# Kernel optimization log

Hardware: AMD Instinct MI355X
Metric: run time of the kernel (lower is better)

## Reference

```python
import jax, jax.numpy as jnp
import numpy as np

NEG_SLOPE = 0.2

def setup_inputs() -> dict:
    key = jax.random.key(0)
    ks = jax.random.split(key, 10)
    N, E, L, D, H = 100000, 3200000, 200000, 128, 128
    x = jax.random.normal(ks[0], (N, D), dtype=jnp.float32)
    edge_index = jax.random.randint(ks[1], (2, E), 0, N, dtype=jnp.int64)
    edge_label_index = jax.random.randint(ks[2], (2, L), 0, N, dtype=jnp.int64)
    s = 1.0 / np.sqrt(D)
    W1l = jax.random.uniform(ks[3], (D, H), minval=-s, maxval=s, dtype=jnp.float32)
    b1 = jax.random.uniform(ks[4], (H,), minval=-s, maxval=s, dtype=jnp.float32)
    W1r = jax.random.uniform(ks[5], (D, H), minval=-s, maxval=s, dtype=jnp.float32)
    s2 = 1.0 / np.sqrt(H)
    W2l = jax.random.uniform(ks[6], (H, H), minval=-s2, maxval=s2, dtype=jnp.float32)
    b2 = jax.random.uniform(ks[7], (H,), minval=-s2, maxval=s2, dtype=jnp.float32)
    W2r = jax.random.uniform(ks[8], (H, H), minval=-s2, maxval=s2, dtype=jnp.float32)
    return {"x": x, "edge_index": edge_index, "edge_label_index": edge_label_index,
            "W1l": W1l, "b1": b1, "W1r": W1r, "W2l": W2l, "b2": b2, "W2r": W2r}

def reference(x, edge_index, edge_label_index, W1l, b1, W1r, W2l, b2, W2r):
    N = x.shape[0]
    src, dst = edge_index[0], edge_index[1]
    # in-degree for mean aggregation (clamped to avoid div-by-zero, matching mean over empty = 0)
    deg = jax.ops.segment_sum(jnp.ones_like(dst, dtype=x.dtype), dst, num_segments=N)
    inv_deg = (1.0 / jnp.maximum(deg, 1.0))[:, None]

    def sage(h, Wl, b, Wr):
        # mean of source-node features over incoming edges at each target node
        agg = jax.ops.segment_sum(h[src], dst, num_segments=N) * inv_deg
        return agg @ Wl + b + h @ Wr

    h = sage(x, W1l, b1, W1r)
    h = jnp.where(h >= 0, h, NEG_SLOPE * h)  # leaky_relu; eval mode so no dropout
    h = sage(h, W2l, b2, W2r)
    x_src = h[edge_label_index[0]]
    x_trg = h[edge_label_index[1]]
    return jnp.sum(x_src * x_trg, axis=1)
```

## Files before the change

kernel.cpp:

```cpp
#include <hip/hip_runtime.h>
#include <hip/hip_fp16.h>


#define D128 128
#define BSHIFT 9
#define BNODES 512

typedef __bf16 bf16x8 __attribute__((ext_vector_type(8)));
typedef float  f32x4  __attribute__((ext_vector_type(4)));
typedef _Float16 h2   __attribute__((ext_vector_type(2)));

union uh2cast { unsigned u; h2 h; };
__device__ inline h2 uash2(unsigned u) { uh2cast c; c.u = u; return c.h; }

__device__ inline unsigned short f2bf(float f) {
    unsigned u = __float_as_uint(f);
    u = u + 0x7FFF + ((u >> 16) & 1);
    return (unsigned short)(u >> 16);
}
__device__ inline float bf2f(unsigned short s) {
    return __uint_as_float(((unsigned)s) << 16);
}
__device__ inline unsigned packbf2(float lo, float hi) {
    return (unsigned)f2bf(lo) | ((unsigned)f2bf(hi) << 16);
}
__device__ inline unsigned char f2e5(float f) {
    unsigned short h = __half_as_ushort(__float2half(f));
    h = (unsigned short)(h + 0x7F + ((h >> 8) & 1));
    return (unsigned char)(h >> 8);
}


__global__ void prep_kernel(const float* __restrict__ in, unsigned short* __restrict__ outb,
                            unsigned char* __restrict__ out8, int n4,
                            const float* __restrict__ W1l, const float* __restrict__ W1r,
                            const float* __restrict__ W2l, const float* __restrict__ W2r,
                            unsigned short* __restrict__ packed,
                            const int* __restrict__ dst, int* __restrict__ bh,
                            int E, int castBlocks, int histBlocks) {
    int bid = blockIdx.x;
    int t = threadIdx.x;
    if (bid < castBlocks) {
        int i = bid * 256 + t;
        if (i >= n4) return;
        float4 v = ((const float4*)in)[i];
        ushort4 ob;
        ob.x = f2bf(v.x); ob.y = f2bf(v.y); ob.z = f2bf(v.z); ob.w = f2bf(v.w);
        ((ushort4*)outb)[i] = ob;
        unsigned p = (unsigned)f2e5(v.x) | ((unsigned)f2e5(v.y) << 8) |
                     ((unsigned)f2e5(v.z) << 16) | ((unsigned)f2e5(v.w) << 24);
        ((unsigned*)out8)[i] = p;
    } else if (bid < castBlocks + 256) {
        int tid = (bid - castBlocks) * 256 + t;
        int layer = tid >> 15;
        int r = tid & 32767;
        int j    = r & 7;
        int lane = (r >> 3) & 63;
        int nt   = (r >> 9) & 7;
        int kc   = (r >> 12) & 7;
        int k   = kc * 32 + ((lane >> 4) << 3) + j;
        int col = nt * 16 + (lane & 15);
        const float* Wl = layer ? W2l : W1l;
        const float* Wr = layer ? W2r : W1r;
        float v = (k < 128) ? Wl[k * 128 + col] : Wr[(k - 128) * 128 + col];
        packed[tid] = f2bf(v);
    } else {
        __shared__ int h[256];
        int hb = bid - castBlocks - 256;
        if (hb >= histBlocks) return;
        h[t] = 0;
        __syncthreads();
        int base = hb * 8192;
#pragma unroll
        for (int k = 0; k < 32; ++k) {
            int e = base + k * 256 + t;
            if (e < E) atomicAdd(&h[dst[e] >> BSHIFT], 1);
        }
        __syncthreads();
        bh[hb * 256 + t] = h[t];
    }
}


__global__ void bucket_scan(const int* __restrict__ bh, int nhb,
                            int* __restrict__ bucket_base, int* __restrict__ bucket_cur,
                            int* __restrict__ rowptr, int NB, int N, int E) {
    __shared__ int sc[256];
    __shared__ int orig[256];
    int t = threadIdx.x;
    int v = 0;
    for (int b = 0; b < nhb; ++b) v += bh[b * 256 + t];
    if (t >= NB) v = 0;
    orig[t] = v;
    sc[t] = v;
    __syncthreads();
    for (int off = 1; off < 256; off <<= 1) {
        int a = (t >= off) ? sc[t - off] : 0;
        __syncthreads();
        sc[t] += a;
        __syncthreads();
    }
    int ex = sc[t] - orig[t];
    if (t < NB) { bucket_base[t] = ex; bucket_cur[t] = ex; }
    if (t == 0) { bucket_base[NB] = E; rowptr[N] = E; }
}

__global__ void scatter_kernel(const int* __restrict__ src, const int* __restrict__ dst,
                               int* __restrict__ bucket_cur, int* __restrict__ pairs,
                               int E, int NB) {
    __shared__ int hist[256], lscan[256], gbase[256];
    __shared__ int lsrc[1024], ldst[1024];
    int t = threadIdx.x;
    hist[t] = 0;
    __syncthreads();
    int base = blockIdx.x * 1024;
    int total = E - base; if (total > 1024) total = 1024;

    int ms[4], md[4], mb[4], mr[4];
#pragma unroll
    for (int k = 0; k < 4; ++k) {
        int i = k * 256 + t;
        int e = base + i;
        mb[k] = -1;
        if (i < total) {
            ms[k] = src[e];
            md[k] = dst[e];
            mb[k] = md[k] >> BSHIFT;
            mr[k] = atomicAdd(&hist[mb[k]], 1);
        }
    }
    __syncthreads();
    lscan[t] = hist[t];
    __syncthreads();
    for (int off = 1; off < 256; off <<= 1) {
        int a = (t >= off) ? lscan[t - off] : 0;
        __syncthreads();
        lscan[t] += a;
        __syncthreads();
    }
    lscan[t] -= hist[t];
    if (t < NB && hist[t] > 0) gbase[t] = atomicAdd(&bucket_cur[t], hist[t]);
    __syncthreads();
#pragma unroll
    for (int k = 0; k < 4; ++k) {
        if (mb[k] >= 0) {
            int idx = lscan[mb[k]] + mr[k];
            lsrc[idx] = ms[k];
            ldst[idx] = md[k];
        }
    }
    __syncthreads();
#pragma unroll
    for (int k = 0; k < 4; ++k) {
        int i = k * 256 + t;
        if (i < total) {
            int d = ldst[i];
            int b = d >> BSHIFT;
            int pos = gbase[b] + (i - lscan[b]);
            pairs[pos] = (lsrc[i] << BSHIFT) | (d & (BNODES - 1));
        }
    }
}

__global__ void bucket_fill(const int* __restrict__ pairs, const int* __restrict__ bucket_base,
                            int* __restrict__ rowptr, int* __restrict__ srcs, int N) {
    __shared__ int hist[BNODES], excl[BNODES], sc[BNODES];
    int b = blockIdx.x;
    int t = threadIdx.x;
    int node0 = b << BSHIFT;
    int pbeg = bucket_base[b];
    int pend = bucket_base[b + 1];
    hist[t] = 0;
    __syncthreads();
    for (int p = pbeg + t; p < pend; p += BNODES) {
        atomicAdd(&hist[pairs[p] & (BNODES - 1)], 1);
    }
    __syncthreads();
    sc[t] = hist[t];
    __syncthreads();
    for (int off = 1; off < BNODES; off <<= 1) {
        int a = (t >= off) ? sc[t - off] : 0;
        __syncthreads();
        sc[t] += a;
        __syncthreads();
    }
    excl[t] = sc[t] - hist[t];
    int node = node0 + t;
    if (node < N) rowptr[node] = pbeg + excl[t];
    __syncthreads();
    hist[t] = 0;
    __syncthreads();
    for (int p = pbeg + t; p < pend; p += BNODES) {
        int w = pairs[p];
        int dl = w & (BNODES - 1);
        int c = atomicAdd(&hist[dl], 1);
        srcs[pbeg + excl[dl] + c] = (int)(((unsigned)w) >> BSHIFT) << 4;
    }
}


__device__ inline void pkacc8(h2* A, uint2 v) {
    A[0] += uash2((v.x << 8) & 0xFF00FF00u);
    A[1] += uash2(v.x & 0xFF00FF00u);
    A[2] += uash2((v.y << 8) & 0xFF00FF00u);
    A[3] += uash2(v.y & 0xFF00FF00u);
}

__global__ void agg_kernel(const int* __restrict__ rowptr, const int* __restrict__ srcs,
                           const unsigned char* __restrict__ feat8,
                           unsigned short* __restrict__ out, int N) {
    int wave = threadIdx.x >> 6;
    int lane = threadIdx.x & 63;
    int q  = lane >> 4;
    int ql = lane & 15;
    int n = blockIdx.x * 4 + wave;
    if (n >= N) return;
    int beg = rowptr[n];
    int end = rowptr[n + 1];
    const uint2* f = (const uint2*)feat8;

    h2 A0[4], A1[4], A2[4], A3[4];
    h2 z; z[0] = (_Float16)0.f; z[1] = (_Float16)0.f;
#pragma unroll
    for (int k = 0; k < 4; ++k) { A0[k] = z; A1[k] = z; A2[k] = z; A3[k] = z; }

    int j = beg;
    int pre = (4 - (beg & 3)) & 3;
    if (pre > end - beg) pre = end - beg;
    if (q < pre) {
        uint2 v = f[srcs[j + q] + ql];
        pkacc8(A1, v);
    }
    j += pre;

    for (; j + 16 <= end; j += 16) {
        int4 e = *(const int4*)(srcs + j + 4 * q);
        uint2 v0 = f[e.x + ql];
        uint2 v1 = f[e.y + ql];
        uint2 v2 = f[e.z + ql];
        uint2 v3 = f[e.w + ql];
        pkacc8(A0, v0);
        pkacc8(A1, v1);
        pkacc8(A2, v2);
        pkacc8(A3, v3);
    }
    for (; j + 4 <= end; j += 4) {
        uint2 v = f[srcs[j + q] + ql];
        pkacc8(A0, v);
    }
    int rem = end - j;
    if (q < rem) {
        uint2 v = f[srcs[j + q] + ql];
        pkacc8(A2, v);
    }

    float c[8];
#pragma unroll
    for (int p = 0; p < 4; ++p) {
        float lo = (float)A0[p][0] + (float)A1[p][0] + (float)A2[p][0] + (float)A3[p][0];
        float hi = (float)A0[p][1] + (float)A1[p][1] + (float)A2[p][1] + (float)A3[p][1];
        int base = (p >> 1) * 4 + (p & 1);
        c[base] = lo;
        c[base + 2] = hi;
    }

#pragma unroll
    for (int k = 0; k < 8; ++k) {
        c[k] += __shfl_xor(c[k], 16, 64);
        c[k] += __shfl_xor(c[k], 32, 64);
    }

    int deg = end - beg;
    float inv = deg > 0 ? 1.0f / (float)deg : 0.f;
    if (q == 0) {
        uint4 r;
        r.x = packbf2(c[0] * inv, c[1] * inv);
        r.y = packbf2(c[2] * inv, c[3] * inv);
        r.z = packbf2(c[4] * inv, c[5] * inv);
        r.w = packbf2(c[6] * inv, c[7] * inv);
        ((uint4*)out)[(size_t)n * 16 + ql] = r;
    }
}


template <bool LEAKY>
__global__ void mm_kernel(const unsigned short* __restrict__ A,
                          const unsigned short* __restrict__ F,
                          const unsigned short* __restrict__ Wp,
                          const float* __restrict__ bias,
                          unsigned short* __restrict__ out,
                          unsigned char* __restrict__ out8, int N) {
    int wid = threadIdx.x >> 6;
    int lane = threadIdx.x & 63;
    int quad = lane >> 4;
    int m0 = (blockIdx.x * 4 + wid) * 32;

    int rowA0 = m0 + (lane & 15);
    int rowA1 = rowA0 + 16;
    if (rowA0 > N - 1) rowA0 = N - 1;
    if (rowA1 > N - 1) rowA1 = N - 1;

    f32x4 acc[2][8];
#pragma unroll
    for (int t = 0; t < 2; ++t)
#pragma unroll
        for (int nt = 0; nt < 8; ++nt) acc[t][nt] = (f32x4){0.f, 0.f, 0.f, 0.f};

#pragma unroll
    for (int kc = 0; kc < 8; ++kc) {
        const unsigned short* src = (kc < 4) ? (A + kc * 32) : (F + (kc - 4) * 32);
        bf16x8 af0 = *(const bf16x8*)(src + (size_t)rowA0 * D128 + quad * 8);
        bf16x8 af1 = *(const bf16x8*)(src + (size_t)rowA1 * D128 + quad * 8);
        const unsigned short* wp = Wp + ((size_t)kc * 8) * 512 + lane * 8;
#pragma unroll
        for (int nt = 0; nt < 8; ++nt) {
            bf16x8 bf = *(const bf16x8*)(wp + nt * 512);
            acc[0][nt] = __builtin_amdgcn_mfma_f32_16x16x32_bf16(af0, bf, acc[0][nt], 0, 0, 0);
            acc[1][nt] = __builtin_amdgcn_mfma_f32_16x16x32_bf16(af1, bf, acc[1][nt], 0, 0, 0);
        }
    }

#pragma unroll
    for (int nt = 0; nt < 8; ++nt) {
        int col = nt * 16 + (lane & 15);
        float bv = bias[col];
#pragma unroll
        for (int t = 0; t < 2; ++t) {
#pragma unroll
            for (int r = 0; r < 4; ++r) {
                int row = m0 + t * 16 + quad * 4 + r;
                if (row < N) {
                    float v = acc[t][nt][r] + bv;
                    if (LEAKY) v = v >= 0.f ? v : 0.2f * v;
                    out[(size_t)row * D128 + col] = f2bf(v);
                    if (out8) out8[(size_t)row * D128 + col] = f2e5(v);
                }
            }
        }
    }
}


__global__ void score_kernel(const int* __restrict__ eli, const unsigned short* __restrict__ h,
                             float* __restrict__ out, int L) {
    int wave = threadIdx.x >> 6;
    int lane = threadIdx.x & 63;
    int l0 = (blockIdx.x * 4 + wave) * 4;
    if (l0 >= L) return;
    const ushort2* h2p = (const ushort2*)h;
    int a[4], b[4];
#pragma unroll
    for (int k = 0; k < 4; ++k) {
        int l = l0 + k;
        if (l > L - 1) l = L - 1;
        a[k] = eli[l];
        b[k] = eli[L + l];
    }
    float p[4];
#pragma unroll
    for (int k = 0; k < 4; ++k) {
        ushort2 u = h2p[(size_t)a[k] * 64 + lane];
        ushort2 v = h2p[(size_t)b[k] * 64 + lane];
        p[k] = bf2f(u.x) * bf2f(v.x) + bf2f(u.y) * bf2f(v.y);
    }
#pragma unroll
    for (int off = 32; off > 0; off >>= 1) {
#pragma unroll
        for (int k = 0; k < 4; ++k) p[k] += __shfl_down(p[k], off, 64);
    }
    if (lane == 0) {
#pragma unroll
        for (int k = 0; k < 4; ++k) {
            if (l0 + k < L) out[l0 + k] = p[k];
        }
    }
}


extern "C" void kernel_launch(void* const* d_in, const int* in_sizes, int n_in,
                              void* d_out, int out_size, void* d_ws, size_t ws_size,
                              hipStream_t stream) {
    const float* x   = (const float*)d_in[0];
    const int*   ei  = (const int*)d_in[1];
    const int*   eli = (const int*)d_in[2];
    const float* W1l = (const float*)d_in[3];
    const float* b1  = (const float*)d_in[4];
    const float* W1r = (const float*)d_in[5];
    const float* W2l = (const float*)d_in[6];
    const float* b2  = (const float*)d_in[7];
    const float* W2r = (const float*)d_in[8];

    const int N = in_sizes[0] / D128;
    const int E = in_sizes[1] / 2;
    const int L = in_sizes[2] / 2;
    const int* srcp = ei;
    const int* dstp = ei + E;
    const int NB = (N + BNODES - 1) >> BSHIFT;

    char* ws = (char*)d_ws;
    size_t off = 0;
    auto alloc = [&](size_t bytes) -> void* {
        void* p = ws + off;
        off += (bytes + 255) & ~(size_t)255;
        return p;
    };
    const int histBlocks = (E + 8191) / 8192;
    int*   rowptr = (int*)alloc((size_t)(N + 1) * sizeof(int));
    int*   bh     = (int*)alloc((size_t)histBlocks * 256 * sizeof(int));
    int*   bbase  = (int*)alloc(257 * sizeof(int));
    int*   bcur   = (int*)alloc(256 * sizeof(int));
    int*   pairs  = (int*)alloc((size_t)E * sizeof(int));
    int*   srcs   = (int*)alloc(((size_t)E + 16) * sizeof(int));
    unsigned short* xb   = (unsigned short*)alloc((size_t)N * D128 * 2);
    unsigned char*  x8   = (unsigned char*)alloc((size_t)N * D128);
    unsigned char*  h1f8 = (unsigned char*)alloc((size_t)N * D128);
    unsigned short* aggb = (unsigned short*)alloc((size_t)N * D128 * 2);
    unsigned short* h1b  = (unsigned short*)alloc((size_t)N * D128 * 2);
    unsigned short* h2b  = (unsigned short*)alloc((size_t)N * D128 * 2);
    unsigned short* Wp   = (unsigned short*)alloc(2 * 32768 * 2);
    (void)ws_size; (void)n_in; (void)out_size;

    int n4 = N * D128 / 4;
    int castBlocks = (n4 + 255) / 256;
    prep_kernel<<<castBlocks + 256 + histBlocks, 256, 0, stream>>>(
        x, xb, x8, n4, W1l, W1r, W2l, W2r, Wp, dstp, bh, E, castBlocks, histBlocks);

    bucket_scan<<<1, 256, 0, stream>>>(bh, histBlocks, bbase, bcur, rowptr, NB, N, E);
    scatter_kernel<<<(E + 1023) / 1024, 256, 0, stream>>>(srcp, dstp, bcur, pairs, E, NB);
    bucket_fill<<<NB, BNODES, 0, stream>>>(pairs, bbase, rowptr, srcs, N);

    agg_kernel<<<(N + 3) / 4, 256, 0, stream>>>(rowptr, srcs, x8, aggb, N);
    mm_kernel<true><<<(N + 127) / 128, 256, 0, stream>>>(aggb, xb, Wp, b1, h1b, h1f8, N);

    agg_kernel<<<(N + 3) / 4, 256, 0, stream>>>(rowptr, srcs, h1f8, aggb, N);
    mm_kernel<false><<<(N + 127) / 128, 256, 0, stream>>>(aggb, h1b, Wp + 32768, b2, h2b,
                                                          (unsigned char*)nullptr, N);

    score_kernel<<<(L + 15) / 16, 256, 0, stream>>>(eli, h2b, (float*)d_out, L);
}
```

Baseline: 510.9 us.

## Use hardware bf8 convert, unroll bucket histogram sum, drop aligned int4 edge loads

Three changes. The fp8 (e5m2) conversion uses the hardware cvt_pk_bf8 builtin when it is available, replacing the integer rounding sequence. The bucket scan sums per-block histograms with eight independent accumulators to expose more memory-level parallelism. The aggregation loop drops the alignment prologue and its int4 index loads and uses four scalar strided index loads instead, which gives a different edge-to-lane assignment and rounding order.

```diff
diff --git a/kernel.cpp b/kernel.cpp
--- a/kernel.cpp
+++ b/kernel.cpp
@@ -25,9 +25,13 @@
     return (unsigned)f2bf(lo) | ((unsigned)f2bf(hi) << 16);
 }
 __device__ inline unsigned char f2e5(float f) {
+#if __has_builtin(__builtin_amdgcn_cvt_pk_bf8_f32)
+    return (unsigned char)(__builtin_amdgcn_cvt_pk_bf8_f32(f, f, 0, false) & 0xFF);
+#else
     unsigned short h = __half_as_ushort(__float2half(f));
     h = (unsigned short)(h + 0x7F + ((h >> 8) & 1));
     return (unsigned char)(h >> 8);
+#endif
 }
 
 
@@ -88,8 +92,20 @@
     __shared__ int sc[256];
     __shared__ int orig[256];
     int t = threadIdx.x;
-    int v = 0;
-    for (int b = 0; b < nhb; ++b) v += bh[b * 256 + t];
+    int a0 = 0, a1 = 0, a2 = 0, a3 = 0, a4 = 0, a5 = 0, a6 = 0, a7 = 0;
+    int b = 0;
+    for (; b + 8 <= nhb; b += 8) {
+        a0 += bh[(b + 0) * 256 + t];
+        a1 += bh[(b + 1) * 256 + t];
+        a2 += bh[(b + 2) * 256 + t];
+        a3 += bh[(b + 3) * 256 + t];
+        a4 += bh[(b + 4) * 256 + t];
+        a5 += bh[(b + 5) * 256 + t];
+        a6 += bh[(b + 6) * 256 + t];
+        a7 += bh[(b + 7) * 256 + t];
+    }
+    for (; b < nhb; ++b) a0 += bh[b * 256 + t];
+    int v = ((a0 + a1) + (a2 + a3)) + ((a4 + a5) + (a6 + a7));
     if (t >= NB) v = 0;
     orig[t] = v;
     sc[t] = v;
@@ -225,20 +241,15 @@
     for (int k = 0; k < 4; ++k) { A0[k] = z; A1[k] = z; A2[k] = z; A3[k] = z; }
 
     int j = beg;
-    int pre = (4 - (beg & 3)) & 3;
-    if (pre > end - beg) pre = end - beg;
-    if (q < pre) {
-        uint2 v = f[srcs[j + q] + ql];
-        pkacc8(A1, v);
-    }
-    j += pre;
-
     for (; j + 16 <= end; j += 16) {
-        int4 e = *(const int4*)(srcs + j + 4 * q);
-        uint2 v0 = f[e.x + ql];
-        uint2 v1 = f[e.y + ql];
-        uint2 v2 = f[e.z + ql];
-        uint2 v3 = f[e.w + ql];
+        int e0 = srcs[j + q];
+        int e1 = srcs[j + 4 + q];
+        int e2 = srcs[j + 8 + q];
+        int e3 = srcs[j + 12 + q];
+        uint2 v0 = f[e0 + ql];
+        uint2 v1 = f[e1 + ql];
+        uint2 v2 = f[e2 + ql];
+        uint2 v3 = f[e3 + ql];
         pkacc8(A0, v0);
         pkacc8(A1, v1);
         pkacc8(A2, v2);
@@ -251,7 +262,7 @@
     int rem = end - j;
     if (q < rem) {
         uint2 v = f[srcs[j + q] + ql];
-        pkacc8(A2, v);
+        pkacc8(A1, v);
     }
 
     float c[8];
```

Measured after the change: 461.0 us. 1.11x faster.
